# Kernel optimization log

Measured on AMD Instinct MI355X. Metric: run time of the kernel, lower is better.

The kernel has to match this reference:

```python
import jax, jax.numpy as jnp
import numpy as np

BOUND = 1.0
MIN_NEAR = 0.2
T_THRESH = 1e-4
MAX_STEPS = 128


def _near_far(rays_o, rays_d):
    # ray-AABB intersection with [-BOUND, BOUND]^3 (near_far_from_aabb)
    d = jnp.where(jnp.abs(rays_d) < 1e-9, 1e-9, rays_d)
    t1 = (-BOUND - rays_o) / d
    t2 = (BOUND - rays_o) / d
    near = jnp.max(jnp.minimum(t1, t2), axis=-1)
    far = jnp.min(jnp.maximum(t1, t2), axis=-1)
    near = jnp.maximum(near, MIN_NEAR)
    far = jnp.maximum(far, near)
    return near, far


def _sample_triplane(planes, pts):
    # planes: [3, C, RES, RES]; pts: [N, 3] in [-1, 1] -> feats [N, 3C]
    def bil(plane, uv):
        res = plane.shape[-1]
        xy = (uv + 1.0) * 0.5 * (res - 1)
        x0 = jnp.clip(jnp.floor(xy).astype(jnp.int32), 0, res - 2)
        w = xy - x0
        wx, wy = w[:, 0], w[:, 1]
        xi, yi = x0[:, 0], x0[:, 1]
        f00 = plane[:, yi, xi]
        f01 = plane[:, yi, xi + 1]
        f10 = plane[:, yi + 1, xi]
        f11 = plane[:, yi + 1, xi + 1]
        f = (f00 * (1 - wx) * (1 - wy) + f01 * wx * (1 - wy)
             + f10 * (1 - wx) * wy + f11 * wx * wy)
        return f.T  # [N, C]
    uvs = (pts[:, jnp.array([0, 1])], pts[:, jnp.array([0, 2])], pts[:, jnp.array([1, 2])])
    return jnp.concatenate([bil(planes[p], uvs[p]) for p in range(3)], axis=-1)


def _forward(rays_o, rays_d, code, density_grid, grid_size, W1, b1, W2, b2, W3, b3):
    S, R, _ = rays_o.shape
    K = MAX_STEPS
    near, far = _near_far(rays_o, rays_d)
    t = (jnp.arange(K, dtype=rays_o.dtype) + 0.5) / K
    z = near[..., None] + (far - near)[..., None] * t            # [S,R,K]
    delta = (far - near) / K                                     # [S,R]
    xyz = rays_o[:, :, None, :] + rays_d[:, :, None, :] * z[..., None]
    xyz = jnp.clip(xyz, -BOUND, BOUND)                           # [S,R,K,3]
    # occupancy-grid masking (density bitfield lookup)
    idx = jnp.clip(((xyz + BOUND) / (2 * BOUND) * grid_size).astype(jnp.int32), 0, grid_size - 1)
    occ = jax.vmap(lambda g, i: g[i[..., 0], i[..., 1], i[..., 2]])(density_grid, idx) > 0  # [S,R,K]
    # point decode: triplane features + small MLP -> (sigma, rgb)
    pts = (xyz / BOUND).reshape(S, R * K, 3)
    feats = jax.vmap(_sample_triplane)(code, pts)                # [S,R*K,96]
    h = jax.nn.relu(feats @ W1 + b1)
    h = jax.nn.relu(h @ W2 + b2)
    out = h @ W3 + b3
    sigma = jax.nn.softplus(out[..., 0]).reshape(S, R, K) * occ.astype(rays_o.dtype)
    rgb = jax.nn.sigmoid(out[..., 1:]).reshape(S, R, K, 3)
    # alpha compositing with early termination at T_thresh
    tau = sigma * delta[..., None]
    T = jnp.exp(-jnp.concatenate([jnp.zeros_like(tau[..., :1]), jnp.cumsum(tau, axis=-1)[..., :-1]], axis=-1))
    alpha = 1.0 - jnp.exp(-tau)
    w = jnp.where(T > T_THRESH, alpha * T, 0.0)
    weights_sum = w.sum(-1)                                      # [S,R]
    depth = (w * z).sum(-1)                                      # [S,R]
    image = (w[..., None] * rgb).sum(-2)                         # [S,R,3]
    return weights_sum, depth, image


def setup_inputs():
    key = jax.random.key(0)
    ks = jax.random.split(key, 8)
    S, R, C, RES, G, H = 4, 2048, 32, 128, 128, 128
    o = jax.random.normal(ks[0], (S, R, 3), jnp.float32)
    rays_o = o / (jnp.linalg.norm(o, axis=-1, keepdims=True) + 1e-6) * 2.5
    d = -rays_o + 0.3 * jax.random.normal(ks[1], (S, R, 3), jnp.float32)
    rays_d = d / (jnp.linalg.norm(d, axis=-1, keepdims=True) + 1e-6)
    code = 0.1 * jax.random.normal(ks[2], (S, 3, C, RES, RES), jnp.float32)
    density_grid = jnp.ones((S, G, G, G), jnp.int32)
    din = 3 * C
    W1 = jax.random.normal(ks[3], (din, H), jnp.float32) / np.sqrt(din).astype(np.float32)
    b1 = jnp.zeros((H,), jnp.float32)
    W2 = jax.random.normal(ks[4], (H, H), jnp.float32) / np.sqrt(H).astype(np.float32)
    b2 = jnp.zeros((H,), jnp.float32)
    W3 = jax.random.normal(ks[5], (H, 4), jnp.float32) / np.sqrt(H).astype(np.float32)
    b3 = jnp.zeros((4,), jnp.float32)
    return {"rays_o": rays_o, "rays_d": rays_d, "code": code, "density_grid": density_grid,
            "grid_size": G, "W1": W1, "b1": b1, "W2": W2, "b2": b2, "W3": W3, "b3": b3}


def reference(rays_o, rays_d, code, density_grid, grid_size, W1, b1, W2, b2, W3, b3):
    return _forward(rays_o, rays_d, code, density_grid, grid_size, W1, b1, W2, b2, W3, b3)
```

## Files before the change

kernel.cpp:

```cpp
#include <hip/hip_runtime.h>
#include <math.h>

#define S_ 4
#define R_ 2048
#define K_ 128
#define C_ 32
#define RES_ 128
#define G_ 128
#define H_ 128

typedef __bf16 bf16x8 __attribute__((ext_vector_type(8)));
typedef float f32x4 __attribute__((ext_vector_type(4)));
typedef float f32x2 __attribute__((ext_vector_type(2)));
typedef unsigned short u16x8 __attribute__((ext_vector_type(8)));

#define CODET_OFF 0
#define CODET_SZ  (S_*3*RES_*RES_*C_/2)
#define W1F_OFF   (CODET_OFF + CODET_SZ)
#define W1F_SZ    (128*96/2)
#define W2F_OFF   (W1F_OFF + W1F_SZ)
#define W2F_SZ    (128*128/2)
#define GB_OFF    (W2F_OFF + W2F_SZ)
#define GB_SZ     (S_*G_*G_*G_/32)
#define SR_OFF    (GB_OFF + GB_SZ)

#define ROWP 136

__device__ __forceinline__ unsigned short f2bf(float x) {
  unsigned int u = __float_as_uint(x);
  unsigned int r = u + 0x7fffu + ((u >> 16) & 1u);
  return (unsigned short)(r >> 16);
}

__global__ __launch_bounds__(256) void k_pre(
    const float* __restrict__ src, unsigned short* __restrict__ dst,
    const int* __restrict__ dgrid, unsigned int* __restrict__ gbits,
    const float* __restrict__ W1, const float* __restrict__ W2,
    unsigned short* __restrict__ W1F, unsigned short* __restrict__ W2F) {
  __shared__ float tile[32 * 65];
  const int t = threadIdx.x;
  const int b = blockIdx.x;
  if (b < 3072) {
    const int slab = b >> 8;
    const int xy0 = (b & 255) << 6;
    const float* sp = src + slab * (C_ * RES_ * RES_);
    unsigned short* dp = dst + slab * (RES_ * RES_ * C_);
    const int i = t & 63, cg = t >> 6;
#pragma unroll
    for (int j = 0; j < 8; ++j) {
      int c = cg * 8 + j;
      tile[c * 65 + i] = sp[c * (RES_ * RES_) + xy0 + i];
    }
    __syncthreads();
    const int i2 = t >> 2, sub = t & 3;
    u16x8 pk;
#pragma unroll
    for (int j = 0; j < 8; ++j) pk[j] = f2bf(tile[(sub * 8 + j) * 65 + i2]);
    *(u16x8*)(dp + (xy0 + i2) * C_ + sub * 8) = pk;
  } else if (b < 4096) {
    const int wi = (b - 3072) * 256 + t;
    const int base = wi * 32;
    unsigned int m = 0;
#pragma unroll 8
    for (int j = 0; j < 32; ++j) m |= (dgrid[base + j] > 0 ? (1u << j) : 0u);
    gbits[wi] = m;
  } else {
    const int slice = b - 4096;
    for (int i = slice * 256 + t; i < 128 * 96; i += 16 * 256) {
      const int j = i & 7, lane = (i >> 3) & 63, fi = i >> 9;
      const int nt = fi / 3, kt = fi - 3 * nt;
      const int k = kt * 32 + (lane >> 4) * 8 + j;
      const int n = nt * 16 + (lane & 15);
      W1F[i] = f2bf(W1[k * H_ + n]);
    }
    for (int i = slice * 256 + t; i < 128 * 128; i += 16 * 256) {
      const int j = i & 7, lane = (i >> 3) & 63, fi = i >> 9;
      const int nt = fi >> 2, kt = fi & 3;
      const int k = kt * 32 + (lane >> 4) * 8 + j;
      const int n = nt * 16 + (lane & 15);
      W2F[i] = f2bf(W2[k * H_ + n]);
    }
  }
}

__device__ __forceinline__ void near_far(float ox, float oy, float oz,
                                         float dx, float dy, float dz,
                                         float& nearv, float& farv) {
  float ddx = fabsf(dx) < 1e-9f ? 1e-9f : dx;
  float ddy = fabsf(dy) < 1e-9f ? 1e-9f : dy;
  float ddz = fabsf(dz) < 1e-9f ? 1e-9f : dz;
  float ix = 1.f / ddx, iy = 1.f / ddy, iz = 1.f / ddz;
  float t1x = (-1.f - ox) * ix, t2x = (1.f - ox) * ix;
  float t1y = (-1.f - oy) * iy, t2y = (1.f - oy) * iy;
  float t1z = (-1.f - oz) * iz, t2z = (1.f - oz) * iz;
  float mnx = fminf(t1x, t2x), mxx = fmaxf(t1x, t2x);
  float mny = fminf(t1y, t2y), mxy = fmaxf(t1y, t2y);
  float mnz = fminf(t1z, t2z), mxz = fmaxf(t1z, t2z);
  nearv = fmaxf(fmaxf(fmaxf(mnx, mny), mnz), 0.2f);
  farv = fmaxf(fminf(fminf(mxx, mxy), mxz), nearv);
}

__global__ __launch_bounds__(256, 5) void k_fused(
    const float* __restrict__ rays_o, const float* __restrict__ rays_d,
    const unsigned short* __restrict__ codeT, const unsigned int* __restrict__ gbits,
    const unsigned short* __restrict__ W1F, const float* __restrict__ b1,
    const unsigned short* __restrict__ W2F, const float* __restrict__ b2,
    const float* __restrict__ W3, const float* __restrict__ b3,
    float* __restrict__ sr) {
  __shared__ __align__(16) unsigned short smem[64 * ROWP];
  unsigned short* fA = smem;
  unsigned short* h1s = smem;

  const int t = threadIdx.x;
  const int w = t >> 6, lane = t & 63;
  const int quad = lane >> 4, ln = lane & 15;
  const int p = t >> 2, q = t & 3;
  const int pG0 = blockIdx.x * 64;
  const int s = blockIdx.x >> 12;
  const int r = (blockIdx.x >> 1) & (R_ - 1);
  const int kbase = (blockIdx.x & 1) * 64;

  const float* ob = rays_o + (s * R_ + r) * 3;
  const float* db = rays_d + (s * R_ + r) * 3;
  const float ox = ob[0], oy = ob[1], oz = ob[2];
  const float dx = db[0], dy = db[1], dz = db[2];
  float nearv, farv;
  near_far(ox, oy, oz, dx, dy, dz, nearv, farv);

  const int q_s = ln & 3, rr_s = ln >> 2;
  const int m_o = 16 * w + quad * 4 + rr_s;
  unsigned int occword;
  int occbit;
  {
    const float zm = nearv + (farv - nearv) * ((kbase + m_o + 0.5f) * (1.0f / K_));
    const float pxm = fminf(fmaxf(ox + dx * zm, -1.f), 1.f);
    const float pym = fminf(fmaxf(oy + dy * zm, -1.f), 1.f);
    const float pzm = fminf(fmaxf(oz + dz * zm, -1.f), 1.f);
    const int i0 = min((int)((pxm + 1.f) * 64.f), G_ - 1);
    const int i1 = min((int)((pym + 1.f) * 64.f), G_ - 1);
    const int i2 = min((int)((pzm + 1.f) * 64.f), G_ - 1);
    const int bidx = ((s * G_ + i0) * G_ + i1) * G_ + i2;
    occword = gbits[bidx >> 5];
    occbit = bidx & 31;
  }

  const float zs = nearv + (farv - nearv) * ((kbase + p + 0.5f) * (1.0f / K_));
  const float px = fminf(fmaxf(ox + dx * zs, -1.f), 1.f);
  const float py = fminf(fmaxf(oy + dy * zs, -1.f), 1.f);
  const float pz = fminf(fmaxf(oz + dz * zs, -1.f), 1.f);

  float w00a, w01a, w10a, w11a, w00b, w01b, w10b, w11b, w00c, w01c, w10c, w11c;
  int off0, off1, off2;
  {
    float fx = (px + 1.f) * 0.5f * 127.f, fy = (py + 1.f) * 0.5f * 127.f;
    int xi = min((int)fx, RES_ - 2), yi = min((int)fy, RES_ - 2);
    float wx = fx - (float)xi, wy = fy - (float)yi;
    w00a = (1.f - wx) * (1.f - wy); w01a = wx * (1.f - wy);
    w10a = (1.f - wx) * wy;         w11a = wx * wy;
    off0 = ((s * 3 + 0) * (RES_ * RES_) + yi * RES_ + xi) * C_;
  }
  {
    float fx = (px + 1.f) * 0.5f * 127.f, fy = (pz + 1.f) * 0.5f * 127.f;
    int xi = min((int)fx, RES_ - 2), yi = min((int)fy, RES_ - 2);
    float wx = fx - (float)xi, wy = fy - (float)yi;
    w00b = (1.f - wx) * (1.f - wy); w01b = wx * (1.f - wy);
    w10b = (1.f - wx) * wy;         w11b = wx * wy;
    off1 = ((s * 3 + 1) * (RES_ * RES_) + yi * RES_ + xi) * C_;
  }
  {
    float fx = (py + 1.f) * 0.5f * 127.f, fy = (pz + 1.f) * 0.5f * 127.f;
    int xi = min((int)fx, RES_ - 2), yi = min((int)fy, RES_ - 2);
    float wx = fx - (float)xi, wy = fy - (float)yi;
    w00c = (1.f - wx) * (1.f - wy); w01c = wx * (1.f - wy);
    w10c = (1.f - wx) * wy;         w11c = wx * wy;
    off2 = ((s * 3 + 2) * (RES_ * RES_) + yi * RES_ + xi) * C_;
  }

#pragma unroll
  for (int u = 0; u < 3; ++u) {
    const int f = 24 * q + 8 * u;
    const int pl = f >> 5;
    const int c = f & 31;
    const int off = (pl == 0) ? off0 : ((pl == 1) ? off1 : off2);
    const float W00 = (pl == 0) ? w00a : ((pl == 1) ? w00b : w00c);
    const float W01 = (pl == 0) ? w01a : ((pl == 1) ? w01b : w01c);
    const float W10 = (pl == 0) ? w10a : ((pl == 1) ? w10b : w10c);
    const float W11 = (pl == 0) ? w11a : ((pl == 1) ? w11b : w11c);
    const unsigned short* bp = codeT + off + c;
    const uint4 A = *(const uint4*)(bp);
    const uint4 B = *(const uint4*)(bp + C_);
    const uint4 Cv = *(const uint4*)(bp + RES_ * C_);
    const uint4 D = *(const uint4*)(bp + RES_ * C_ + C_);
    const unsigned int aw[4] = {A.x, A.y, A.z, A.w};
    const unsigned int bw[4] = {B.x, B.y, B.z, B.w};
    const unsigned int cw[4] = {Cv.x, Cv.y, Cv.z, Cv.w};
    const unsigned int dw[4] = {D.x, D.y, D.z, D.w};
    const f32x2 W00v = {W00, W00}, W01v = {W01, W01}, W10v = {W10, W10}, W11v = {W11, W11};
    unsigned int ow[4];
#pragma unroll
    for (int e2 = 0; e2 < 4; ++e2) {
      const f32x2 va = {__uint_as_float(aw[e2] << 16), __uint_as_float(aw[e2] & 0xffff0000u)};
      const f32x2 vb = {__uint_as_float(bw[e2] << 16), __uint_as_float(bw[e2] & 0xffff0000u)};
      const f32x2 vc = {__uint_as_float(cw[e2] << 16), __uint_as_float(cw[e2] & 0xffff0000u)};
      const f32x2 vd = {__uint_as_float(dw[e2] << 16), __uint_as_float(dw[e2] & 0xffff0000u)};
      const f32x2 fv = W00v * va + W01v * vb + W10v * vc + W11v * vd;
      ow[e2] = __builtin_amdgcn_perm(__float_as_uint(fv[1]), __float_as_uint(fv[0]),
                                     0x07060302u);
    }
    *(uint4*)(fA + p * ROWP + f) = make_uint4(ow[0], ow[1], ow[2], ow[3]);
  }

  f32x4 acc[8];
#pragma unroll
  for (int nt = 0; nt < 8; ++nt) acc[nt] = (f32x4){0.f, 0.f, 0.f, 0.f};
  {
    bf16x8 afr[3];
#pragma unroll
    for (int kt = 0; kt < 3; ++kt)
      afr[kt] = *(const bf16x8*)(fA + (16 * w + ln) * ROWP + kt * 32 + quad * 8);
#pragma unroll
    for (int nt = 0; nt < 8; ++nt) {
      const bf16x8 b0 = *(const bf16x8*)(W1F + ((nt * 3 + 0) * 64 + lane) * 8);
      const bf16x8 b1v = *(const bf16x8*)(W1F + ((nt * 3 + 1) * 64 + lane) * 8);
      const bf16x8 b2v = *(const bf16x8*)(W1F + ((nt * 3 + 2) * 64 + lane) * 8);
      acc[nt] = __builtin_amdgcn_mfma_f32_16x16x32_bf16(afr[0], b0, acc[nt], 0, 0, 0);
      acc[nt] = __builtin_amdgcn_mfma_f32_16x16x32_bf16(afr[1], b1v, acc[nt], 0, 0, 0);
      acc[nt] = __builtin_amdgcn_mfma_f32_16x16x32_bf16(afr[2], b2v, acc[nt], 0, 0, 0);
    }
#pragma unroll
    for (int nt = 0; nt < 8; ++nt) {
      const int n = nt * 16 + ln;
      const float bias = b1[n];
#pragma unroll
      for (int rr = 0; rr < 4; ++rr) {
        const int m = 16 * w + quad * 4 + rr;
        const float v = fmaxf(acc[nt][rr] + bias, 0.f);
        h1s[m * ROWP + n] = (unsigned short)(__float_as_uint(v) >> 16);
      }
    }
  }

#pragma unroll
  for (int nt = 0; nt < 8; ++nt) acc[nt] = (f32x4){0.f, 0.f, 0.f, 0.f};
  {
    bf16x8 afr[4];
#pragma unroll
    for (int kt = 0; kt < 4; ++kt)
      afr[kt] = *(const bf16x8*)(h1s + (16 * w + ln) * ROWP + kt * 32 + quad * 8);
#pragma unroll
    for (int nt = 0; nt < 8; ++nt) {
      const bf16x8 b0 = *(const bf16x8*)(W2F + ((nt * 4 + 0) * 64 + lane) * 8);
      const bf16x8 b1v = *(const bf16x8*)(W2F + ((nt * 4 + 1) * 64 + lane) * 8);
      const bf16x8 b2v = *(const bf16x8*)(W2F + ((nt * 4 + 2) * 64 + lane) * 8);
      const bf16x8 b3v = *(const bf16x8*)(W2F + ((nt * 4 + 3) * 64 + lane) * 8);
      acc[nt] = __builtin_amdgcn_mfma_f32_16x16x32_bf16(afr[0], b0, acc[nt], 0, 0, 0);
      acc[nt] = __builtin_amdgcn_mfma_f32_16x16x32_bf16(afr[1], b1v, acc[nt], 0, 0, 0);
      acc[nt] = __builtin_amdgcn_mfma_f32_16x16x32_bf16(afr[2], b2v, acc[nt], 0, 0, 0);
      acc[nt] = __builtin_amdgcn_mfma_f32_16x16x32_bf16(afr[3], b3v, acc[nt], 0, 0, 0);
    }
  }

  float part[4][4];
#pragma unroll
  for (int rr = 0; rr < 4; ++rr)
#pragma unroll
    for (int qq = 0; qq < 4; ++qq) part[rr][qq] = 0.f;
#pragma unroll
  for (int nt = 0; nt < 8; ++nt) {
    const int n = nt * 16 + ln;
    const float b2n = b2[n];
    const float4 w3v = *(const float4*)(W3 + n * 4);
#pragma unroll
    for (int rr = 0; rr < 4; ++rr) {
      const float hv = fmaxf(acc[nt][rr] + b2n, 0.f);
      part[rr][0] = fmaf(hv, w3v.x, part[rr][0]);
      part[rr][1] = fmaf(hv, w3v.y, part[rr][1]);
      part[rr][2] = fmaf(hv, w3v.z, part[rr][2]);
      part[rr][3] = fmaf(hv, w3v.w, part[rr][3]);
    }
  }
  float v16[16];
#pragma unroll
  for (int rr = 0; rr < 4; ++rr)
#pragma unroll
    for (int qq = 0; qq < 4; ++qq) v16[rr * 4 + qq] = part[rr][qq];
  float v8[8];
#pragma unroll
  for (int j = 0; j < 8; ++j) {
    const float a = v16[2 * j], c = v16[2 * j + 1];
    const float send = (ln & 1) ? a : c;
    const float keep = (ln & 1) ? c : a;
    v8[j] = keep + __shfl_xor(send, 1);
  }
  float v4a[4];
#pragma unroll
  for (int j = 0; j < 4; ++j) {
    const float a = v8[2 * j], c = v8[2 * j + 1];
    const float send = (ln & 2) ? a : c;
    const float keep = (ln & 2) ? c : a;
    v4a[j] = keep + __shfl_xor(send, 2);
  }
  float v2a[2];
#pragma unroll
  for (int j = 0; j < 2; ++j) {
    const float a = v4a[2 * j], c = v4a[2 * j + 1];
    const float send = (ln & 4) ? a : c;
    const float keep = (ln & 4) ? c : a;
    v2a[j] = keep + __shfl_xor(send, 4);
  }
  float v1;
  {
    const float a = v2a[0], c = v2a[1];
    const float send = (ln & 8) ? a : c;
    const float keep = (ln & 8) ? c : a;
    v1 = keep + __shfl_xor(send, 8);
  }

  const float val = v1 + b3[q_s];

  float outv;
  if (q_s == 0) {
    const int occ = (occword >> occbit) & 1;
    const float sp = val > 20.f ? val : log1pf(expf(val));
    outv = occ ? sp : 0.f;
  } else {
    outv = 1.f / (1.f + expf(-val));
  }
  sr[(pG0 + m_o) * 4 + q_s] = outv;
}

__global__ __launch_bounds__(256) void k_render(
    const float* __restrict__ rays_o, const float* __restrict__ rays_d,
    const float4* __restrict__ sr4, float* __restrict__ out) {
  const int lane = threadIdx.x & 63;
  const int ray = blockIdx.x * 4 + (threadIdx.x >> 6);
  const int s = ray >> 11, r = ray & (R_ - 1);
  const float* ob = rays_o + (s * R_ + r) * 3;
  const float* db = rays_d + (s * R_ + r) * 3;
  float nearv, farv;
  near_far(ob[0], ob[1], ob[2], db[0], db[1], db[2], nearv, farv);
  const float delta = (farv - nearv) * (1.0f / K_);

  const int k0 = lane * 2;
  const float4 A = sr4[ray * K_ + k0];
  const float4 B = sr4[ray * K_ + k0 + 1];
  const float tau0 = A.x * delta, tau1 = B.x * delta;
  const float local = tau0 + tau1;
  float scan = local;
#pragma unroll
  for (int off = 1; off < 64; off <<= 1) {
    const float vsh = __shfl_up(scan, off);
    if (lane >= off) scan += vsh;
  }
  const float pre = scan - local;
  const float T0 = expf(-pre);
  const float T1 = expf(-(pre + tau0));
  const float a0 = 1.f - expf(-tau0);
  const float a1 = 1.f - expf(-tau1);
  const float w0 = (T0 > 1e-4f) ? a0 * T0 : 0.f;
  const float w1 = (T1 > 1e-4f) ? a1 * T1 : 0.f;
  const float z0 = nearv + (farv - nearv) * ((k0 + 0.5f) * (1.f / K_));
  const float z1 = nearv + (farv - nearv) * ((k0 + 1.5f) * (1.f / K_));

  float sw = w0 + w1;
  float sd = w0 * z0 + w1 * z1;
  float sred = w0 * A.y + w1 * B.y;
  float sgrn = w0 * A.z + w1 * B.z;
  float sblu = w0 * A.w + w1 * B.w;
#pragma unroll
  for (int mk = 32; mk >= 1; mk >>= 1) {
    sw += __shfl_xor(sw, mk);
    sd += __shfl_xor(sd, mk);
    sred += __shfl_xor(sred, mk);
    sgrn += __shfl_xor(sgrn, mk);
    sblu += __shfl_xor(sblu, mk);
  }
  if (lane == 0) {
    out[ray] = sw;
    out[S_ * R_ + ray] = sd;
    out[2 * S_ * R_ + ray * 3 + 0] = sred;
    out[2 * S_ * R_ + ray * 3 + 1] = sgrn;
    out[2 * S_ * R_ + ray * 3 + 2] = sblu;
  }
}

extern "C" void kernel_launch(void* const* d_in, const int* in_sizes, int n_in,
                              void* d_out, int out_size, void* d_ws, size_t ws_size,
                              hipStream_t stream) {
  const float* rays_o = (const float*)d_in[0];
  const float* rays_d = (const float*)d_in[1];
  const float* code = (const float*)d_in[2];
  const int* dgrid = (const int*)d_in[3];
  const float* W1 = (const float*)d_in[5];
  const float* b1 = (const float*)d_in[6];
  const float* W2 = (const float*)d_in[7];
  const float* b2 = (const float*)d_in[8];
  const float* W3 = (const float*)d_in[9];
  const float* b3 = (const float*)d_in[10];

  float* ws = (float*)d_ws;
  unsigned short* codeT = (unsigned short*)(ws + CODET_OFF);
  unsigned short* W1F = (unsigned short*)(ws + W1F_OFF);
  unsigned short* W2F = (unsigned short*)(ws + W2F_OFF);
  unsigned int* gbits = (unsigned int*)(ws + GB_OFF);
  float* sr = ws + SR_OFF;

  hipLaunchKernelGGL(k_pre, dim3(4112), dim3(256), 0, stream,
                     code, codeT, dgrid, gbits, W1, W2, W1F, W2F);
  hipLaunchKernelGGL(k_fused, dim3((S_ * R_ * K_) / 64), dim3(256), 0, stream,
                     rays_o, rays_d, codeT, gbits, W1F, b1, W2F, b2, W3, b3, sr);
  hipLaunchKernelGGL(k_render, dim3((S_ * R_) / 4), dim3(256), 0, stream,
                     rays_o, rays_d, (const float4*)sr, (float*)d_out);
}
```

Before: 304.1 us.

## Process a whole ray per block with two MFMA row tiles per wave; ballot-pack grid bits

k_fused now assigns one full ray (128 samples) to each 256-thread block instead of 64 samples. Each wave computes two 16-row M tiles, so every W1/W2 B-fragment loaded from global memory feeds two MFMAs. The layer-2 accumulators are consumed per n-tile, removing the 8-tile accumulator array. The density bitfield pack in k_pre now uses wave ballots over coalesced loads instead of per-thread strided 32-element loops. In exchange, LDS per block doubles and the occupancy hint drops from 5 to 4 blocks per CU.

```diff
diff --git a/kernel.cpp b/kernel.cpp
--- a/kernel.cpp
+++ b/kernel.cpp
@@ -58,12 +58,17 @@
     for (int j = 0; j < 8; ++j) pk[j] = f2bf(tile[(sub * 8 + j) * 65 + i2]);
     *(u16x8*)(dp + (xy0 + i2) * C_ + sub * 8) = pk;
   } else if (b < 4096) {
-    const int wi = (b - 3072) * 256 + t;
-    const int base = wi * 32;
-    unsigned int m = 0;
-#pragma unroll 8
-    for (int j = 0; j < 32; ++j) m |= (dgrid[base + j] > 0 ? (1u << j) : 0u);
-    gbits[wi] = m;
+    const int base0 = (b - 3072) * 8192;
+    const int lane = t & 63;
+#pragma unroll 4
+    for (int j = 0; j < 32; ++j) {
+      const int idx = base0 + j * 256 + t;
+      const unsigned long long m = __ballot(dgrid[idx] > 0);
+      if (lane == 0)
+        gbits[idx >> 5] = (unsigned int)m;
+      else if (lane == 32)
+        gbits[idx >> 5] = (unsigned int)(m >> 32);
+    }
   } else {
     const int slice = b - 4096;
     for (int i = slice * 256 + t; i < 128 * 96; i += 16 * 256) {
@@ -100,39 +105,75 @@
   farv = fmaxf(fminf(fminf(mxx, mxy), mxz), nearv);
 }
 
-__global__ __launch_bounds__(256, 5) void k_fused(
+__device__ __forceinline__ float reduce16(const float (&part)[4][4], const int ln) {
+  float v16[16];
+#pragma unroll
+  for (int rr = 0; rr < 4; ++rr)
+#pragma unroll
+    for (int qq = 0; qq < 4; ++qq) v16[rr * 4 + qq] = part[rr][qq];
+  float v8[8];
+#pragma unroll
+  for (int j = 0; j < 8; ++j) {
+    const float a = v16[2 * j], c = v16[2 * j + 1];
+    const float send = (ln & 1) ? a : c;
+    const float keep = (ln & 1) ? c : a;
+    v8[j] = keep + __shfl_xor(send, 1);
+  }
+  float v4a[4];
+#pragma unroll
+  for (int j = 0; j < 4; ++j) {
+    const float a = v8[2 * j], c = v8[2 * j + 1];
+    const float send = (ln & 2) ? a : c;
+    const float keep = (ln & 2) ? c : a;
+    v4a[j] = keep + __shfl_xor(send, 2);
+  }
+  float v2a[2];
+#pragma unroll
+  for (int j = 0; j < 2; ++j) {
+    const float a = v4a[2 * j], c = v4a[2 * j + 1];
+    const float send = (ln & 4) ? a : c;
+    const float keep = (ln & 4) ? c : a;
+    v2a[j] = keep + __shfl_xor(send, 4);
+  }
+  const float a = v2a[0], c = v2a[1];
+  const float send = (ln & 8) ? a : c;
+  const float keep = (ln & 8) ? c : a;
+  return keep + __shfl_xor(send, 8);
+}
+
+__global__ __launch_bounds__(256, 4) void k_fused(
     const float* __restrict__ rays_o, const float* __restrict__ rays_d,
     const unsigned short* __restrict__ codeT, const unsigned int* __restrict__ gbits,
     const unsigned short* __restrict__ W1F, const float* __restrict__ b1,
     const unsigned short* __restrict__ W2F, const float* __restrict__ b2,
     const float* __restrict__ W3, const float* __restrict__ b3,
     float* __restrict__ sr) {
-  __shared__ __align__(16) unsigned short smem[64 * ROWP];
+  __shared__ __align__(16) unsigned short smem[128 * ROWP];
   unsigned short* fA = smem;
   unsigned short* h1s = smem;
 
   const int t = threadIdx.x;
   const int w = t >> 6, lane = t & 63;
   const int quad = lane >> 4, ln = lane & 15;
-  const int p = t >> 2, q = t & 3;
-  const int pG0 = blockIdx.x * 64;
-  const int s = blockIdx.x >> 12;
-  const int r = (blockIdx.x >> 1) & (R_ - 1);
-  const int kbase = (blockIdx.x & 1) * 64;
-
-  const float* ob = rays_o + (s * R_ + r) * 3;
-  const float* db = rays_d + (s * R_ + r) * 3;
+  const int p = t >> 1, q = t & 1;
+  const int ray = blockIdx.x;
+  const int s = ray >> 11;
+  const int pG0 = ray * K_;
+
+  const float* ob = rays_o + ray * 3;
+  const float* db = rays_d + ray * 3;
   const float ox = ob[0], oy = ob[1], oz = ob[2];
   const float dx = db[0], dy = db[1], dz = db[2];
   float nearv, farv;
   near_far(ox, oy, oz, dx, dy, dz, nearv, farv);
 
   const int q_s = ln & 3, rr_s = ln >> 2;
-  const int m_o = 16 * w + quad * 4 + rr_s;
-  unsigned int occword;
-  int occbit;
-  {
-    const float zm = nearv + (farv - nearv) * ((kbase + m_o + 0.5f) * (1.0f / K_));
+  const int m_o0 = 32 * w + quad * 4 + rr_s;
+  const int m_o1 = m_o0 + 16;
+  unsigned int occw0, occw1;
+  int occb0, occb1;
+  {
+    const float zm = nearv + (farv - nearv) * ((m_o0 + 0.5f) * (1.0f / K_));
     const float pxm = fminf(fmaxf(ox + dx * zm, -1.f), 1.f);
     const float pym = fminf(fmaxf(oy + dy * zm, -1.f), 1.f);
     const float pzm = fminf(fmaxf(oz + dz * zm, -1.f), 1.f);
@@ -140,11 +181,23 @@
     const int i1 = min((int)((pym + 1.f) * 64.f), G_ - 1);
     const int i2 = min((int)((pzm + 1.f) * 64.f), G_ - 1);
     const int bidx = ((s * G_ + i0) * G_ + i1) * G_ + i2;
-    occword = gbits[bidx >> 5];
-    occbit = bidx & 31;
-  }
-
-  const float zs = nearv + (farv - nearv) * ((kbase + p + 0.5f) * (1.0f / K_));
+    occw0 = gbits[bidx >> 5];
+    occb0 = bidx & 31;
+  }
+  {
+    const float zm = nearv + (farv - nearv) * ((m_o1 + 0.5f) * (1.0f / K_));
+    const float pxm = fminf(fmaxf(ox + dx * zm, -1.f), 1.f);
+    const float pym = fminf(fmaxf(oy + dy * zm, -1.f), 1.f);
+    const float pzm = fminf(fmaxf(oz + dz * zm, -1.f), 1.f);
+    const int i0 = min((int)((pxm + 1.f) * 64.f), G_ - 1);
+    const int i1 = min((int)((pym + 1.f) * 64.f), G_ - 1);
+    const int i2 = min((int)((pzm + 1.f) * 64.f), G_ - 1);
+    const int bidx = ((s * G_ + i0) * G_ + i1) * G_ + i2;
+    occw1 = gbits[bidx >> 5];
+    occb1 = bidx & 31;
+  }
+
+  const float zs = nearv + (farv - nearv) * ((p + 0.5f) * (1.0f / K_));
   const float px = fminf(fmaxf(ox + dx * zs, -1.f), 1.f);
   const float py = fminf(fmaxf(oy + dy * zs, -1.f), 1.f);
   const float pz = fminf(fmaxf(oz + dz * zs, -1.f), 1.f);
@@ -177,8 +230,8 @@
   }
 
 #pragma unroll
-  for (int u = 0; u < 3; ++u) {
-    const int f = 24 * q + 8 * u;
+  for (int u = 0; u < 6; ++u) {
+    const int f = 48 * q + 8 * u;
     const int pl = f >> 5;
     const int c = f & 31;
     const int off = (pl == 0) ? off0 : ((pl == 1) ? off1 : off2);
@@ -210,123 +263,117 @@
     *(uint4*)(fA + p * ROWP + f) = make_uint4(ow[0], ow[1], ow[2], ow[3]);
   }
 
-  f32x4 acc[8];
-#pragma unroll
-  for (int nt = 0; nt < 8; ++nt) acc[nt] = (f32x4){0.f, 0.f, 0.f, 0.f};
-  {
-    bf16x8 afr[3];
-#pragma unroll
-    for (int kt = 0; kt < 3; ++kt)
-      afr[kt] = *(const bf16x8*)(fA + (16 * w + ln) * ROWP + kt * 32 + quad * 8);
+  const int rowA = 32 * w + ln;
+  const int rowB = rowA + 16;
+
+  {
+    bf16x8 aA[3], aB[3];
+#pragma unroll
+    for (int kt = 0; kt < 3; ++kt) {
+      aA[kt] = *(const bf16x8*)(fA + rowA * ROWP + kt * 32 + quad * 8);
+      aB[kt] = *(const bf16x8*)(fA + rowB * ROWP + kt * 32 + quad * 8);
+    }
 #pragma unroll
     for (int nt = 0; nt < 8; ++nt) {
       const bf16x8 b0 = *(const bf16x8*)(W1F + ((nt * 3 + 0) * 64 + lane) * 8);
       const bf16x8 b1v = *(const bf16x8*)(W1F + ((nt * 3 + 1) * 64 + lane) * 8);
       const bf16x8 b2v = *(const bf16x8*)(W1F + ((nt * 3 + 2) * 64 + lane) * 8);
-      acc[nt] = __builtin_amdgcn_mfma_f32_16x16x32_bf16(afr[0], b0, acc[nt], 0, 0, 0);
-      acc[nt] = __builtin_amdgcn_mfma_f32_16x16x32_bf16(afr[1], b1v, acc[nt], 0, 0, 0);
-      acc[nt] = __builtin_amdgcn_mfma_f32_16x16x32_bf16(afr[2], b2v, acc[nt], 0, 0, 0);
-    }
-#pragma unroll
-    for (int nt = 0; nt < 8; ++nt) {
+      f32x4 accA = {0.f, 0.f, 0.f, 0.f};
+      f32x4 accB = {0.f, 0.f, 0.f, 0.f};
+      accA = __builtin_amdgcn_mfma_f32_16x16x32_bf16(aA[0], b0, accA, 0, 0, 0);
+      accB = __builtin_amdgcn_mfma_f32_16x16x32_bf16(aB[0], b0, accB, 0, 0, 0);
+      accA = __builtin_amdgcn_mfma_f32_16x16x32_bf16(aA[1], b1v, accA, 0, 0, 0);
+      accB = __builtin_amdgcn_mfma_f32_16x16x32_bf16(aB[1], b1v, accB, 0, 0, 0);
+      accA = __builtin_amdgcn_mfma_f32_16x16x32_bf16(aA[2], b2v, accA, 0, 0, 0);
+      accB = __builtin_amdgcn_mfma_f32_16x16x32_bf16(aB[2], b2v, accB, 0, 0, 0);
       const int n = nt * 16 + ln;
       const float bias = b1[n];
 #pragma unroll
       for (int rr = 0; rr < 4; ++rr) {
-        const int m = 16 * w + quad * 4 + rr;
-        const float v = fmaxf(acc[nt][rr] + bias, 0.f);
-        h1s[m * ROWP + n] = (unsigned short)(__float_as_uint(v) >> 16);
+        const int mA = 32 * w + quad * 4 + rr;
+        const float vA = fmaxf(accA[rr] + bias, 0.f);
+        h1s[mA * ROWP + n] = (unsigned short)(__float_as_uint(vA) >> 16);
+        const float vB = fmaxf(accB[rr] + bias, 0.f);
+        h1s[(mA + 16) * ROWP + n] = (unsigned short)(__float_as_uint(vB) >> 16);
       }
     }
   }
 
-#pragma unroll
-  for (int nt = 0; nt < 8; ++nt) acc[nt] = (f32x4){0.f, 0.f, 0.f, 0.f};
-  {
-    bf16x8 afr[4];
-#pragma unroll
-    for (int kt = 0; kt < 4; ++kt)
-      afr[kt] = *(const bf16x8*)(h1s + (16 * w + ln) * ROWP + kt * 32 + quad * 8);
+  float part0[4][4], part1[4][4];
+#pragma unroll
+  for (int rr = 0; rr < 4; ++rr)
+#pragma unroll
+    for (int qq = 0; qq < 4; ++qq) {
+      part0[rr][qq] = 0.f;
+      part1[rr][qq] = 0.f;
+    }
+  {
+    bf16x8 aA[4], aB[4];
+#pragma unroll
+    for (int kt = 0; kt < 4; ++kt) {
+      aA[kt] = *(const bf16x8*)(h1s + rowA * ROWP + kt * 32 + quad * 8);
+      aB[kt] = *(const bf16x8*)(h1s + rowB * ROWP + kt * 32 + quad * 8);
+    }
 #pragma unroll
     for (int nt = 0; nt < 8; ++nt) {
       const bf16x8 b0 = *(const bf16x8*)(W2F + ((nt * 4 + 0) * 64 + lane) * 8);
       const bf16x8 b1v = *(const bf16x8*)(W2F + ((nt * 4 + 1) * 64 + lane) * 8);
       const bf16x8 b2v = *(const bf16x8*)(W2F + ((nt * 4 + 2) * 64 + lane) * 8);
       const bf16x8 b3v = *(const bf16x8*)(W2F + ((nt * 4 + 3) * 64 + lane) * 8);
-      acc[nt] = __builtin_amdgcn_mfma_f32_16x16x32_bf16(afr[0], b0, acc[nt], 0, 0, 0);
-      acc[nt] = __builtin_amdgcn_mfma_f32_16x16x32_bf16(afr[1], b1v, acc[nt], 0, 0, 0);
-      acc[nt] = __builtin_amdgcn_mfma_f32_16x16x32_bf16(afr[2], b2v, acc[nt], 0, 0, 0);
-      acc[nt] = __builtin_amdgcn_mfma_f32_16x16x32_bf16(afr[3], b3v, acc[nt], 0, 0, 0);
-    }
-  }
-
-  float part[4][4];
-#pragma unroll
-  for (int rr = 0; rr < 4; ++rr)
-#pragma unroll
-    for (int qq = 0; qq < 4; ++qq) part[rr][qq] = 0.f;
-#pragma unroll
-  for (int nt = 0; nt < 8; ++nt) {
-    const int n = nt * 16 + ln;
-    const float b2n = b2[n];
-    const float4 w3v = *(const float4*)(W3 + n * 4);
-#pragma unroll
-    for (int rr = 0; rr < 4; ++rr) {
-      const float hv = fmaxf(acc[nt][rr] + b2n, 0.f);
-      part[rr][0] = fmaf(hv, w3v.x, part[rr][0]);
-      part[rr][1] = fmaf(hv, w3v.y, part[rr][1]);
-      part[rr][2] = fmaf(hv, w3v.z, part[rr][2]);
-      part[rr][3] = fmaf(hv, w3v.w, part[rr][3]);
-    }
-  }
-  float v16[16];
-#pragma unroll
-  for (int rr = 0; rr < 4; ++rr)
-#pragma unroll
-    for (int qq = 0; qq < 4; ++qq) v16[rr * 4 + qq] = part[rr][qq];
-  float v8[8];
-#pragma unroll
-  for (int j = 0; j < 8; ++j) {
-    const float a = v16[2 * j], c = v16[2 * j + 1];
-    const float send = (ln & 1) ? a : c;
-    const float keep = (ln & 1) ? c : a;
-    v8[j] = keep + __shfl_xor(send, 1);
-  }
-  float v4a[4];
-#pragma unroll
-  for (int j = 0; j < 4; ++j) {
-    const float a = v8[2 * j], c = v8[2 * j + 1];
-    const float send = (ln & 2) ? a : c;
-    const float keep = (ln & 2) ? c : a;
-    v4a[j] = keep + __shfl_xor(send, 2);
-  }
-  float v2a[2];
-#pragma unroll
-  for (int j = 0; j < 2; ++j) {
-    const float a = v4a[2 * j], c = v4a[2 * j + 1];
-    const float send = (ln & 4) ? a : c;
-    const float keep = (ln & 4) ? c : a;
-    v2a[j] = keep + __shfl_xor(send, 4);
-  }
-  float v1;
-  {
-    const float a = v2a[0], c = v2a[1];
-    const float send = (ln & 8) ? a : c;
-    const float keep = (ln & 8) ? c : a;
-    v1 = keep + __shfl_xor(send, 8);
-  }
-
-  const float val = v1 + b3[q_s];
-
-  float outv;
-  if (q_s == 0) {
-    const int occ = (occword >> occbit) & 1;
-    const float sp = val > 20.f ? val : log1pf(expf(val));
-    outv = occ ? sp : 0.f;
-  } else {
-    outv = 1.f / (1.f + expf(-val));
-  }
-  sr[(pG0 + m_o) * 4 + q_s] = outv;
+      f32x4 accA = {0.f, 0.f, 0.f, 0.f};
+      f32x4 accB = {0.f, 0.f, 0.f, 0.f};
+      accA = __builtin_amdgcn_mfma_f32_16x16x32_bf16(aA[0], b0, accA, 0, 0, 0);
+      accB = __builtin_amdgcn_mfma_f32_16x16x32_bf16(aB[0], b0, accB, 0, 0, 0);
+      accA = __builtin_amdgcn_mfma_f32_16x16x32_bf16(aA[1], b1v, accA, 0, 0, 0);
+      accB = __builtin_amdgcn_mfma_f32_16x16x32_bf16(aB[1], b1v, accB, 0, 0, 0);
+      accA = __builtin_amdgcn_mfma_f32_16x16x32_bf16(aA[2], b2v, accA, 0, 0, 0);
+      accB = __builtin_amdgcn_mfma_f32_16x16x32_bf16(aB[2], b2v, accB, 0, 0, 0);
+      accA = __builtin_amdgcn_mfma_f32_16x16x32_bf16(aA[3], b3v, accA, 0, 0, 0);
+      accB = __builtin_amdgcn_mfma_f32_16x16x32_bf16(aB[3], b3v, accB, 0, 0, 0);
+      const int n = nt * 16 + ln;
+      const float b2n = b2[n];
+      const float4 w3v = *(const float4*)(W3 + n * 4);
+#pragma unroll
+      for (int rr = 0; rr < 4; ++rr) {
+        const float hA = fmaxf(accA[rr] + b2n, 0.f);
+        part0[rr][0] = fmaf(hA, w3v.x, part0[rr][0]);
+        part0[rr][1] = fmaf(hA, w3v.y, part0[rr][1]);
+        part0[rr][2] = fmaf(hA, w3v.z, part0[rr][2]);
+        part0[rr][3] = fmaf(hA, w3v.w, part0[rr][3]);
+        const float hB = fmaxf(accB[rr] + b2n, 0.f);
+        part1[rr][0] = fmaf(hB, w3v.x, part1[rr][0]);
+        part1[rr][1] = fmaf(hB, w3v.y, part1[rr][1]);
+        part1[rr][2] = fmaf(hB, w3v.z, part1[rr][2]);
+        part1[rr][3] = fmaf(hB, w3v.w, part1[rr][3]);
+      }
+    }
+  }
+
+  const float bq = b3[q_s];
+  {
+    const float val = reduce16(part0, ln) + bq;
+    float outv;
+    if (q_s == 0) {
+      const int occ = (occw0 >> occb0) & 1;
+      const float sp = val > 20.f ? val : log1pf(expf(val));
+      outv = occ ? sp : 0.f;
+    } else {
+      outv = 1.f / (1.f + expf(-val));
+    }
+    sr[(pG0 + m_o0) * 4 + q_s] = outv;
+  }
+  {
+    const float val = reduce16(part1, ln) + bq;
+    float outv;
+    if (q_s == 0) {
+      const int occ = (occw1 >> occb1) & 1;
+      const float sp = val > 20.f ? val : log1pf(expf(val));
+      outv = occ ? sp : 0.f;
+    } else {
+      outv = 1.f / (1.f + expf(-val));
+    }
+    sr[(pG0 + m_o1) * 4 + q_s] = outv;
+  }
 }
 
 __global__ __launch_bounds__(256) void k_render(
@@ -407,7 +454,7 @@
 
   hipLaunchKernelGGL(k_pre, dim3(4112), dim3(256), 0, stream,
                      code, codeT, dgrid, gbits, W1, W2, W1F, W2F);
-  hipLaunchKernelGGL(k_fused, dim3((S_ * R_ * K_) / 64), dim3(256), 0, stream,
+  hipLaunchKernelGGL(k_fused, dim3(S_ * R_), dim3(256), 0, stream,
                      rays_o, rays_d, codeT, gbits, W1F, b1, W2F, b2, W3, b3, sr);
   hipLaunchKernelGGL(k_render, dim3((S_ * R_) / 4), dim3(256), 0, stream,
                      rays_o, rays_d, (const float4*)sr, (float*)d_out);
```

After: 282.3 us. -7.2%, faster.
